# Kernel optimization log

Measured on AMD Instinct MI355X. Metric: run time of the kernel, lower is better.

Reference implementation:

```python
import jax, jax.numpy as jnp
import numpy as np

D_H = 2048      # d_hidden
D_E = 1408      # d_expert (per routed expert)
E = 8           # n_routed_experts
K = 2           # n_experts_per_token (top-k)
N_SHARED = 2    # n_shared_experts -> shared expert dim = D_E * N_SHARED
B, S = 1, 2048
D_S = D_E * N_SHARED


def setup_inputs() -> dict:
    key = jax.random.key(0)
    ks = jax.random.split(key, 8)
    def init(k, shape, fan_in):
        # nn.Linear default init: U(-1/sqrt(fan_in), 1/sqrt(fan_in))
        bound = 1.0 / np.sqrt(fan_in)
        return jax.random.uniform(k, shape, jnp.float32, -bound, bound)
    x = jax.random.normal(ks[0], (B, S, D_H), jnp.float32)
    gate_W = init(ks[1], (E, D_H), D_H)          # router: logits = x @ gate_W.T
    Wg_e = init(ks[2], (E, D_E, D_H), D_H)       # per-expert W_gate (out,in)
    Wu_e = init(ks[3], (E, D_E, D_H), D_H)       # per-expert W_up
    Wd_e = init(ks[4], (E, D_H, D_E), D_E)       # per-expert W_down
    Wg_s = init(ks[5], (D_S, D_H), D_H)          # shared expert W_gate
    Wu_s = init(ks[6], (D_S, D_H), D_H)
    Wd_s = init(ks[7], (D_H, D_S), D_S)
    return {"x": x, "gate_W": gate_W, "Wg_e": Wg_e, "Wu_e": Wu_e,
            "Wd_e": Wd_e, "Wg_s": Wg_s, "Wu_s": Wu_s, "Wd_s": Wd_s}


def reference(x, gate_W, Wg_e, Wu_e, Wd_e, Wg_s, Wu_s, Wd_s):
    silu = jax.nn.silu
    # shared expert: SiLU-gated MLP over all tokens
    shared = (silu(x @ Wg_s.T) * (x @ Wu_s.T)) @ Wd_s.T          # [B,S,D_H]
    # gating: softmax over experts, then top-k scores/indices
    scores = jax.nn.softmax(x @ gate_W.T, axis=-1)                # [B,S,E]
    topk_scores, topk_idx = jax.lax.top_k(scores, K)              # [B,S,K]
    # dense combine weights w[t,e] = topk score if e selected else 0
    # (equivalent to the torch argsort-dispatch + scatter_reduce sum combine)
    w = jnp.sum(jax.nn.one_hot(topk_idx, E, dtype=x.dtype) * topk_scores[..., None], axis=-2)  # [B,S,E]
    xf = x.reshape(-1, D_H)                                       # [T,D_H], T = B*S
    wf = w.reshape(-1, E)                                         # [T,E]
    # per-expert SiLU-gated MLP, batched over experts
    g = jnp.einsum('td,efd->etf', xf, Wg_e)                       # [E,T,D_E]
    u = jnp.einsum('td,efd->etf', xf, Wu_e)
    h = silu(g) * u
    oe = jnp.einsum('etf,edf->etd', h, Wd_e)                      # [E,T,D_H]
    routed = jnp.einsum('etd,te->td', oe, wf).reshape(B, S, D_H)
    return routed + shared
```

## Files before the change

### kernel.cpp

```cpp
#include <hip/hip_runtime.h>

using short8 = __attribute__((ext_vector_type(8))) short;
using f32x4  = __attribute__((ext_vector_type(4))) float;
typedef unsigned short ushort_t;
typedef unsigned int u32;

#define T_TOK 2048
#define DH 2048
#define DE 1408
#define DS 2816
#define GU_NB 440
#define DN_NB 256

#define NGEc 23068672UL
#define NGSc 5767168UL
#define PA_CVT_BLOCKS 30208
#define PB_CVT_BLOCKS 7040

__device__ __forceinline__ unsigned short f2bf(float f) {
  unsigned u = __float_as_uint(f);
  u += 0x7FFF + ((u >> 16) & 1);
  return (unsigned short)(u >> 16);
}

__device__ __forceinline__ void gl_lds16(const void* g, void* l) {
  __builtin_amdgcn_global_load_lds((const __attribute__((address_space(1))) u32*)g,
                                   (__attribute__((address_space(3))) u32*)l, 16, 0, 0);
}

__device__ __forceinline__ short8 pack_bf8(float4 a, float4 b) {
  short8 o;
  o[0] = (short)f2bf(a.x); o[1] = (short)f2bf(a.y);
  o[2] = (short)f2bf(a.z); o[3] = (short)f2bf(a.w);
  o[4] = (short)f2bf(b.x); o[5] = (short)f2bf(b.y);
  o[6] = (short)f2bf(b.z); o[7] = (short)f2bf(b.w);
  return o;
}

__global__ void phaseA_kernel(const float* __restrict__ x, const float* __restrict__ gW,
                              int* __restrict__ counts, int* __restrict__ tok_e,
                              int* __restrict__ tok_slot, float* __restrict__ tok_w,
                              const float* __restrict__ Wg_e, const float* __restrict__ Wu_e,
                              const float* __restrict__ Wg_s, const float* __restrict__ Wu_s,
                              ushort_t* wbg_e, ushort_t* wbu_e,
                              ushort_t* wbg_s, ushort_t* wbu_s, ushort_t* xb) {
  int b = blockIdx.x;
  int tid = threadIdx.x;
  if (b < 512) {
    int wid = tid >> 6, lane = tid & 63;
    int t = b * 4 + wid;
    float acc[8] = {0.f,0.f,0.f,0.f,0.f,0.f,0.f,0.f};
    const float* xt = x + (size_t)t * DH;
    for (int i = lane; i < DH; i += 64) {
      float xv = xt[i];
#pragma unroll
      for (int e = 0; e < 8; e++) acc[e] += xv * gW[e * DH + i];
    }
#pragma unroll
    for (int e = 0; e < 8; e++) {
#pragma unroll
      for (int off = 32; off > 0; off >>= 1) acc[e] += __shfl_xor(acc[e], off);
    }
    if (lane == 0) {
      float mx = acc[0];
      for (int e = 1; e < 8; e++) mx = fmaxf(mx, acc[e]);
      float p[8], se = 0.f;
      for (int e = 0; e < 8; e++) { p[e] = __expf(acc[e] - mx); se += p[e]; }
      for (int e = 0; e < 8; e++) p[e] /= se;
      int i1 = 0;
      for (int e = 1; e < 8; e++) if (p[e] > p[i1]) i1 = e;
      int i2 = (i1 == 0) ? 1 : 0;
      for (int e = 0; e < 8; e++) if (e != i1 && p[e] > p[i2]) i2 = e;
      int s1 = atomicAdd(&counts[i1], 1);
      int s2 = atomicAdd(&counts[i2], 1);
      tok_e[2 * t] = i1;     tok_e[2 * t + 1] = i2;
      tok_slot[2 * t] = s1;  tok_slot[2 * t + 1] = s2;
      tok_w[2 * t] = p[i1];  tok_w[2 * t + 1] = p[i2];
    }
    return;
  }
  size_t i = (size_t)(b - 512) * 2048 + (size_t)tid * 8;
  const float* s; ushort_t* d; size_t o;
  if      (i < NGEc)                    { s = Wg_e; d = wbg_e; o = i; }
  else if (i < 2 * NGEc)                { s = Wu_e; d = wbu_e; o = i - NGEc; }
  else if (i < 2 * NGEc + NGSc)         { s = Wg_s; d = wbg_s; o = i - 2 * NGEc; }
  else if (i < 2 * NGEc + 2 * NGSc)     { s = Wu_s; d = wbu_s; o = i - 2 * NGEc - NGSc; }
  else                                  { s = x;    d = xb;    o = i - 2 * NGEc - 2 * NGSc; }
  float4 a = *(const float4*)(s + o);
  float4 bb = *(const float4*)(s + o + 4);
  *(short8*)(d + o) = pack_bf8(a, bb);
}

__global__ void prefix_assign_kernel(const int* __restrict__ counts, int* __restrict__ ebase,
                                     int* __restrict__ gu_off, int* __restrict__ dn_off,
                                     const int* __restrict__ tok_e, int* __restrict__ tok_slot,
                                     int* __restrict__ slot2tok) {
  __shared__ int sbase[8];
  if (threadIdx.x == 0) {
    int a = 0;
    for (int e = 0; e < 8; e++) { sbase[e] = a; ebase[e] = a; a += counts[e]; }
    int g = 0, d = 0;
    for (int z = 0; z < 8; z++) {
      gu_off[z] = g; dn_off[z] = d;
      int Lg = (counts[z] + 255) >> 8;
      g += Lg * 11;
      int Ld = (counts[z] + 255) >> 8;
      d += Ld * 8;
    }
    gu_off[8] = g; g += 88;
    gu_off[9] = g; g += 88;
    gu_off[10] = g;
    dn_off[8] = d; d += 64;
    dn_off[9] = d;
  }
  __syncthreads();
  for (int idx = threadIdx.x; idx < T_TOK * 2; idx += blockDim.x) {
    int e = tok_e[idx];
    int g = sbase[e] + tok_slot[idx];
    tok_slot[idx] = g;
    slot2tok[g] = idx >> 1;
  }
}

__global__ __launch_bounds__(512, 1) void phaseB_kernel(
    const ushort_t* __restrict__ xb, const int* __restrict__ counts,
    const int* __restrict__ ebase, const int* __restrict__ gu_off,
    const int* __restrict__ slot2tok,
    const ushort_t* __restrict__ Wbg_e, const ushort_t* __restrict__ Wbu_e,
    const ushort_t* __restrict__ Wbg_s, const ushort_t* __restrict__ Wbu_s,
    ushort_t* __restrict__ h_r, ushort_t* __restrict__ h_s,
    const float* __restrict__ Wd_e, const float* __restrict__ Wd_s,
    ushort_t* wbd_e, ushort_t* wbd_s) {
  extern __shared__ char smem[];
  int tid = threadIdx.x;
  if (blockIdx.x >= GU_NB) {
    size_t i = (size_t)(blockIdx.x - GU_NB) * 4096 + (size_t)tid * 8;
    const float* s; ushort_t* d; size_t o;
    if (i < NGEc) { s = Wd_e; d = wbd_e; o = i; }
    else          { s = Wd_s; d = wbd_s; o = i - NGEc; }
    float4 a = *(const float4*)(s + o);
    float4 bb = *(const float4*)(s + o + 4);
    *(short8*)(d + o) = pack_bf8(a, bb);
    return;
  }
  int b = blockIdx.x;
  int c = (b & 7) * (GU_NB >> 3) + (b >> 3);
  int off[11];
#pragma unroll
  for (int zz = 0; zz < 11; zz++) off[zz] = gu_off[zz];
  if (c >= off[10]) return;
  int z = 0;
#pragma unroll
  for (int zz = 1; zz < 10; zz++) if (c >= off[zz]) z = zz;
  int cz = c - off[z];

  bool routed = (z < 8);
  int cnt, gbase, Lm;
  const ushort_t *Bg, *Bu;
  if (routed) {
    cnt = counts[z]; gbase = ebase[z];
    Lm = (cnt + 255) >> 8;
    Bg = Wbg_e + (size_t)z * DE * DH;
    Bu = Wbu_e + (size_t)z * DE * DH;
  } else {
    cnt = T_TOK; gbase = 0; Lm = 8;
    Bg = Wbg_s + (size_t)(z - 8) * 1408 * DH;
    Bu = Wbu_s + (size_t)(z - 8) * 1408 * DH;
  }
  int mt = cz % Lm, y = cz / Lm;
  int m0 = mt * 256, n0 = y * 128;

  int lane = tid & 63, w = tid >> 6;
  int lr = lane & 15, lk = lane >> 4;
  int wm = w >> 1, wn = w & 1;

  const ushort_t* asrc[4];
  int adst[4];
#pragma unroll
  for (int j = 0; j < 4; j++) {
    int r = (w * 4 + j) * 8 + (lane >> 3);
    int lrow = m0 + r;
    int tok = routed ? ((lrow < cnt) ? slot2tok[gbase + lrow] : 0) : lrow;
    int cs = (lane & 7) ^ (r & 7);
    asrc[j] = xb + (size_t)tok * DH + cs * 8;
    adst[j] = (w * 4 + j) * 1024;
  }
  const ushort_t* gsrc[2];
  const ushort_t* usrc[2];
  int wdst[2];
#pragma unroll
  for (int j = 0; j < 2; j++) {
    int r = (w * 2 + j) * 8 + (lane >> 3);
    int cs = (lane & 7) ^ (r & 7);
    gsrc[j] = Bg + (size_t)(n0 + r) * DH + cs * 8;
    usrc[j] = Bu + (size_t)(n0 + r) * DH + cs * 8;
    wdst[j] = (w * 2 + j) * 1024;
  }

  f32x4 accg[4][4] = {};
  f32x4 accu[4][4] = {};

#define GU_STAGE(buf, k0)                                             \
  {                                                                   \
    char* ab = smem + (buf) * 32768;                                  \
    char* gb = smem + 65536 + (buf) * 16384;                          \
    char* ub = smem + 98304 + (buf) * 16384;                          \
    _Pragma("unroll")                                                 \
    for (int j = 0; j < 4; j++) gl_lds16(asrc[j] + (k0), ab + adst[j]); \
    _Pragma("unroll")                                                 \
    for (int j = 0; j < 2; j++) {                                     \
      gl_lds16(gsrc[j] + (k0), gb + wdst[j]);                         \
      gl_lds16(usrc[j] + (k0), ub + wdst[j]);                         \
    }                                                                 \
  }

  const int nt = DH >> 6;
  GU_STAGE(0, 0);
  __syncthreads();
  int cur = 0;
  for (int t = 0; t < nt; t++) {
    if (t + 1 < nt) GU_STAGE(cur ^ 1, (t + 1) * 64);
    const char* ab = smem + cur * 32768;
    const char* gb = smem + 65536 + cur * 16384;
    const char* ub = smem + 98304 + cur * 16384;
    short8 af[4][2], bg[4][2], bu[4][2];
#pragma unroll
    for (int m = 0; m < 4; m++) {
#pragma unroll
      for (int ks = 0; ks < 2; ks++) {
        int rr = wm * 64 + m * 16 + lr;
        af[m][ks] = *(const short8*)(ab + rr * 128 + ((ks * 64 + lk * 16) ^ ((rr & 7) << 4)));
      }
    }
#pragma unroll
    for (int n = 0; n < 4; n++) {
#pragma unroll
      for (int ks = 0; ks < 2; ks++) {
        int cc = wn * 64 + n * 16 + lr;
        bg[n][ks] = *(const short8*)(gb + cc * 128 + ((ks * 64 + lk * 16) ^ ((cc & 7) << 4)));
        bu[n][ks] = *(const short8*)(ub + cc * 128 + ((ks * 64 + lk * 16) ^ ((cc & 7) << 4)));
      }
    }
    __builtin_amdgcn_s_setprio(1);
#pragma unroll
    for (int m = 0; m < 4; m++) {
#pragma unroll
      for (int n = 0; n < 4; n++) {
#pragma unroll
        for (int ks = 0; ks < 2; ks++) {
          accg[m][n] = __builtin_amdgcn_mfma_f32_16x16x32_bf16(af[m][ks], bg[n][ks], accg[m][n], 0, 0, 0);
          accu[m][n] = __builtin_amdgcn_mfma_f32_16x16x32_bf16(af[m][ks], bu[n][ks], accu[m][n], 0, 0, 0);
        }
      }
    }
    __builtin_amdgcn_s_setprio(0);
    __syncthreads();
    cur ^= 1;
  }
#pragma unroll
  for (int m = 0; m < 4; m++) {
    int rowl = m0 + wm * 64 + m * 16 + lk * 4;
#pragma unroll
    for (int n = 0; n < 4; n++) {
      int col = n0 + wn * 64 + n * 16 + lr;
#pragma unroll
      for (int j = 0; j < 4; j++) {
        float g = accg[m][n][j], u = accu[m][n][j];
        float s = g / (1.f + __expf(-g));
        unsigned short hv = f2bf(s * u);
        if (routed) {
          if (rowl + j < cnt) h_r[(size_t)(gbase + rowl + j) * DE + col] = hv;
        } else {
          h_s[(size_t)(rowl + j) * DS + (z - 8) * 1408 + col] = hv;
        }
      }
    }
  }
}

__global__ __launch_bounds__(512, 1) void down_kernel(
    const ushort_t* __restrict__ h_r, const ushort_t* __restrict__ h_s,
    const int* __restrict__ counts, const int* __restrict__ ebase,
    const int* __restrict__ dn_off,
    const ushort_t* __restrict__ Wbd_e, const ushort_t* __restrict__ Wbd_s,
    float* __restrict__ oe, float* __restrict__ out) {
  extern __shared__ char smem[];

  int b = blockIdx.x;
  int c = (b & 7) * (DN_NB >> 3) + (b >> 3);
  int off[10];
#pragma unroll
  for (int zz = 0; zz < 10; zz++) off[zz] = dn_off[zz];
  if (c >= off[9]) return;
  int z = 0;
#pragma unroll
  for (int zz = 1; zz < 9; zz++) if (c >= off[zz]) z = zz;
  int cz = c - off[z];

  bool routed = (z < 8);
  int cnt, gbase, K, Lm;
  const ushort_t* Abase;
  const ushort_t* Bw;
  if (routed) {
    cnt = counts[z]; gbase = ebase[z];
    Lm = (cnt + 255) >> 8;
    K = DE;
    Abase = h_r + (size_t)gbase * DE;
    Bw = Wbd_e + (size_t)z * DH * DE;
  } else {
    cnt = T_TOK; gbase = 0; Lm = 8;
    K = DS;
    Abase = h_s;
    Bw = Wbd_s;
  }
  int mt = cz % Lm, y = cz / Lm;
  int m0 = mt * 256, n0 = y * 256;

  int tid = threadIdx.x;
  int lane = tid & 63, w = tid >> 6;
  int lr = lane & 15, lk = lane >> 4;
  int wm = w >> 2, wn = w & 3;

  const ushort_t* asrc[4];
  const ushort_t* bsrc[4];
  int dst4[4];
#pragma unroll
  for (int j = 0; j < 4; j++) {
    int r = (w * 4 + j) * 8 + (lane >> 3);
    int cs = (lane & 7) ^ (r & 7);
    asrc[j] = Abase + (size_t)(m0 + r) * K + cs * 8;
    bsrc[j] = Bw + (size_t)(n0 + r) * K + cs * 8;
    dst4[j] = (w * 4 + j) * 1024;
  }

  f32x4 acc[8][4] = {};

#define DN_STAGE(buf, k0)                                             \
  {                                                                   \
    char* ab = smem + (buf) * 32768;                                  \
    char* wb2 = smem + 65536 + (buf) * 32768;                         \
    _Pragma("unroll")                                                 \
    for (int j = 0; j < 4; j++) {                                     \
      gl_lds16(asrc[j] + (k0), ab + dst4[j]);                         \
      gl_lds16(bsrc[j] + (k0), wb2 + dst4[j]);                        \
    }                                                                 \
  }

  const int nt = K >> 6;
  DN_STAGE(0, 0);
  __syncthreads();
  int cur = 0;
  for (int t = 0; t < nt; t++) {
    if (t + 1 < nt) DN_STAGE(cur ^ 1, (t + 1) * 64);
    const char* ab = smem + cur * 32768;
    const char* wb2 = smem + 65536 + cur * 32768;
    short8 bf[4][2];
#pragma unroll
    for (int n = 0; n < 4; n++) {
#pragma unroll
      for (int ks = 0; ks < 2; ks++) {
        int cc = wn * 64 + n * 16 + lr;
        bf[n][ks] = *(const short8*)(wb2 + cc * 128 + ((ks * 64 + lk * 16) ^ ((cc & 7) << 4)));
      }
    }
    __builtin_amdgcn_s_setprio(1);
#pragma unroll
    for (int mh = 0; mh < 2; mh++) {
      short8 af[4][2];
#pragma unroll
      for (int m4 = 0; m4 < 4; m4++) {
#pragma unroll
        for (int ks = 0; ks < 2; ks++) {
          int rr = wm * 128 + (mh * 4 + m4) * 16 + lr;
          af[m4][ks] = *(const short8*)(ab + rr * 128 + ((ks * 64 + lk * 16) ^ ((rr & 7) << 4)));
        }
      }
#pragma unroll
      for (int m4 = 0; m4 < 4; m4++) {
#pragma unroll
        for (int n = 0; n < 4; n++) {
#pragma unroll
          for (int ks = 0; ks < 2; ks++) {
            acc[mh * 4 + m4][n] = __builtin_amdgcn_mfma_f32_16x16x32_bf16(
                af[m4][ks], bf[n][ks], acc[mh * 4 + m4][n], 0, 0, 0);
          }
        }
      }
    }
    __builtin_amdgcn_s_setprio(0);
    __syncthreads();
    cur ^= 1;
  }
#pragma unroll
  for (int m = 0; m < 8; m++) {
    int rowl = m0 + wm * 128 + m * 16 + lk * 4;
#pragma unroll
    for (int n = 0; n < 4; n++) {
      int col = n0 + wn * 64 + n * 16 + lr;
#pragma unroll
      for (int j = 0; j < 4; j++) {
        if (routed) {
          if (rowl + j < cnt) oe[(size_t)(gbase + rowl + j) * DH + col] = acc[m][n][j];
        } else {
          out[(size_t)(rowl + j) * DH + col] = acc[m][n][j];
        }
      }
    }
  }
}

__global__ void combine_kernel(const int* __restrict__ tok_gslot,
                               const float* __restrict__ tok_w,
                               const float* __restrict__ oe,
                               float* __restrict__ out) {
  int t = blockIdx.x;
  int g1 = tok_gslot[2 * t], g2 = tok_gslot[2 * t + 1];
  float w1 = tok_w[2 * t], w2 = tok_w[2 * t + 1];
  int i = threadIdx.x * 8;
  const float4* p1 = (const float4*)(oe + (size_t)g1 * DH + i);
  const float4* p2 = (const float4*)(oe + (size_t)g2 * DH + i);
  float4* po = (float4*)(out + (size_t)t * DH + i);
  float4 a0 = p1[0], a1 = p1[1];
  float4 b0 = p2[0], b1 = p2[1];
  float4 o0 = po[0], o1 = po[1];
  o0.x += w1 * a0.x + w2 * b0.x;  o0.y += w1 * a0.y + w2 * b0.y;
  o0.z += w1 * a0.z + w2 * b0.z;  o0.w += w1 * a0.w + w2 * b0.w;
  o1.x += w1 * a1.x + w2 * b1.x;  o1.y += w1 * a1.y + w2 * b1.y;
  o1.z += w1 * a1.z + w2 * b1.z;  o1.w += w1 * a1.w + w2 * b1.w;
  po[0] = o0; po[1] = o1;
}

extern "C" void kernel_launch(void* const* d_in, const int* in_sizes, int n_in,
                              void* d_out, int out_size, void* d_ws, size_t ws_size,
                              hipStream_t stream) {
  const float* x    = (const float*)d_in[0];
  const float* gW   = (const float*)d_in[1];
  const float* Wg_e = (const float*)d_in[2];
  const float* Wu_e = (const float*)d_in[3];
  const float* Wd_e = (const float*)d_in[4];
  const float* Wg_s = (const float*)d_in[5];
  const float* Wu_s = (const float*)d_in[6];
  const float* Wd_s = (const float*)d_in[7];
  float* out = (float*)d_out;

  char* ws = (char*)d_ws;
  int*   counts   = (int*)ws;
  int*   ebase    = (int*)(ws + 64);
  int*   gu_off   = (int*)(ws + 128);
  int*   dn_off   = (int*)(ws + 192);
  int*   tok_e    = (int*)(ws + 256);
  int*   tok_slot = (int*)(ws + 256 + 16384);
  float* tok_w    = (float*)(ws + 256 + 32768);
  int*   slot2tok = (int*)(ws + 256 + 49152);
  ushort_t* xb  = (ushort_t*)(ws + 131072);
  ushort_t* h_r = (ushort_t*)(ws + 131072 + (size_t)T_TOK * DH * 2);
  ushort_t* h_s = h_r + (size_t)4096 * DE;
  float*    oe  = (float*)((char*)h_s + (size_t)T_TOK * DS * 2);
  ushort_t* wb  = (ushort_t*)((char*)oe + (size_t)4096 * DH * 4);
  ushort_t* wbg_e = wb;
  ushort_t* wbu_e = wb + NGEc;
  ushort_t* wbd_e = wb + 2 * NGEc;
  ushort_t* wbg_s = wb + 3 * NGEc;
  ushort_t* wbu_s = wbg_s + NGSc;
  ushort_t* wbd_s = wbg_s + 2 * NGSc;

  hipFuncSetAttribute((const void*)phaseB_kernel,
                      hipFuncAttributeMaxDynamicSharedMemorySize, 131072);
  hipFuncSetAttribute((const void*)down_kernel,
                      hipFuncAttributeMaxDynamicSharedMemorySize, 131072);

  hipMemsetAsync(counts, 0, 64, stream);
  phaseA_kernel<<<512 + PA_CVT_BLOCKS, 256, 0, stream>>>(
      x, gW, counts, tok_e, tok_slot, tok_w,
      Wg_e, Wu_e, Wg_s, Wu_s, wbg_e, wbu_e, wbg_s, wbu_s, xb);
  prefix_assign_kernel<<<1, 256, 0, stream>>>(counts, ebase, gu_off, dn_off,
                                              tok_e, tok_slot, slot2tok);
  phaseB_kernel<<<GU_NB + PB_CVT_BLOCKS, 512, 131072, stream>>>(
      xb, counts, ebase, gu_off, slot2tok, wbg_e, wbu_e, wbg_s, wbu_s, h_r, h_s,
      Wd_e, Wd_s, wbd_e, wbd_s);
  down_kernel<<<DN_NB, 512, 131072, stream>>>(
      h_r, h_s, counts, ebase, dn_off, wbd_e, wbd_s, oe, out);
  combine_kernel<<<T_TOK, 256, 0, stream>>>(tok_slot, tok_w, oe, out);
}
```

Before: 343.9 us.

## Split GEMM mainloops into four barrier-synchronized phases with interleaved async loads

```diff
diff --git a/kernel.cpp b/kernel.cpp
--- a/kernel.cpp
+++ b/kernel.cpp
@@ -16,6 +16,8 @@
 #define NGSc 5767168UL
 #define PA_CVT_BLOCKS 30208
 #define PB_CVT_BLOCKS 7040
+
+#define FENCE() asm volatile("" ::: "memory")
 
 __device__ __forceinline__ unsigned short f2bf(float f) {
   unsigned u = __float_as_uint(f);
@@ -174,16 +176,19 @@
   int lr = lane & 15, lk = lane >> 4;
   int wm = w >> 1, wn = w & 1;
 
-  const ushort_t* asrc[4];
-  int adst[4];
-#pragma unroll
-  for (int j = 0; j < 4; j++) {
-    int r = (w * 4 + j) * 8 + (lane >> 3);
-    int lrow = m0 + r;
-    int tok = routed ? ((lrow < cnt) ? slot2tok[gbase + lrow] : 0) : lrow;
-    int cs = (lane & 7) ^ (r & 7);
-    asrc[j] = xb + (size_t)tok * DH + cs * 8;
-    adst[j] = (w * 4 + j) * 1024;
+  const ushort_t* asrc[2][2];
+  int adst[2][2];
+#pragma unroll
+  for (int h = 0; h < 2; h++) {
+#pragma unroll
+    for (int j = 0; j < 2; j++) {
+      int r = h * 128 + (w * 2 + j) * 8 + (lane >> 3);
+      int lrow = m0 + r;
+      int tok = routed ? ((lrow < cnt) ? slot2tok[gbase + lrow] : 0) : lrow;
+      int cs = (lane & 7) ^ (r & 7);
+      asrc[h][j] = xb + (size_t)tok * DH + cs * 8;
+      adst[h][j] = h * 16384 + (w * 2 + j) * 1024;
+    }
   }
   const ushort_t* gsrc[2];
   const ushort_t* usrc[2];
@@ -200,62 +205,82 @@
   f32x4 accg[4][4] = {};
   f32x4 accu[4][4] = {};
 
-#define GU_STAGE(buf, k0)                                             \
-  {                                                                   \
-    char* ab = smem + (buf) * 32768;                                  \
-    char* gb = smem + 65536 + (buf) * 16384;                          \
-    char* ub = smem + 98304 + (buf) * 16384;                          \
-    _Pragma("unroll")                                                 \
-    for (int j = 0; j < 4; j++) gl_lds16(asrc[j] + (k0), ab + adst[j]); \
-    _Pragma("unroll")                                                 \
-    for (int j = 0; j < 2; j++) {                                     \
-      gl_lds16(gsrc[j] + (k0), gb + wdst[j]);                         \
-      gl_lds16(usrc[j] + (k0), ub + wdst[j]);                         \
-    }                                                                 \
-  }
+#define GU_ST_A(p, h, k0)                                              \
+  { char* _d = smem + (p) * 32768;                                     \
+    gl_lds16(asrc[h][0] + (k0), _d + adst[h][0]);                      \
+    gl_lds16(asrc[h][1] + (k0), _d + adst[h][1]); }
+#define GU_ST_G(p, k0)                                                 \
+  { char* _d = smem + 65536 + (p) * 16384;                             \
+    gl_lds16(gsrc[0] + (k0), _d + wdst[0]);                            \
+    gl_lds16(gsrc[1] + (k0), _d + wdst[1]); }
+#define GU_ST_U(p, k0)                                                 \
+  { char* _d = smem + 98304 + (p) * 16384;                             \
+    gl_lds16(usrc[0] + (k0), _d + wdst[0]);                            \
+    gl_lds16(usrc[1] + (k0), _d + wdst[1]); }
 
   const int nt = DH >> 6;
-  GU_STAGE(0, 0);
-  __syncthreads();
-  int cur = 0;
+  GU_ST_A(0, 0, 0); GU_ST_A(0, 1, 0);
+  GU_ST_G(0, 0);    GU_ST_U(0, 0);
+  GU_ST_G(1, 64);   GU_ST_U(1, 64);
+  asm volatile("s_waitcnt vmcnt(4)" ::: "memory");
+  FENCE(); __builtin_amdgcn_s_barrier(); FENCE();
+
+  short8 bfr[4][2];
   for (int t = 0; t < nt; t++) {
-    if (t + 1 < nt) GU_STAGE(cur ^ 1, (t + 1) * 64);
-    const char* ab = smem + cur * 32768;
-    const char* gb = smem + 65536 + cur * 16384;
-    const char* ub = smem + 98304 + cur * 16384;
-    short8 af[4][2], bg[4][2], bu[4][2];
-#pragma unroll
-    for (int m = 0; m < 4; m++) {
-#pragma unroll
-      for (int ks = 0; ks < 2; ks++) {
-        int rr = wm * 64 + m * 16 + lr;
-        af[m][ks] = *(const short8*)(ab + rr * 128 + ((ks * 64 + lk * 16) ^ ((rr & 7) << 4)));
-      }
-    }
-#pragma unroll
-    for (int n = 0; n < 4; n++) {
-#pragma unroll
-      for (int ks = 0; ks < 2; ks++) {
-        int cc = wn * 64 + n * 16 + lr;
-        bg[n][ks] = *(const short8*)(gb + cc * 128 + ((ks * 64 + lk * 16) ^ ((cc & 7) << 4)));
-        bu[n][ks] = *(const short8*)(ub + cc * 128 + ((ks * 64 + lk * 16) ^ ((cc & 7) << 4)));
-      }
-    }
-    __builtin_amdgcn_s_setprio(1);
-#pragma unroll
-    for (int m = 0; m < 4; m++) {
-#pragma unroll
-      for (int n = 0; n < 4; n++) {
+    int p = t & 1;
+    const char* ab = smem + p * 32768;
+    const char* gb = smem + 65536 + p * 16384;
+    const char* ub = smem + 98304 + p * 16384;
+    int k1 = (t + 1) * 64, k2 = (t + 2) * 64;
+#pragma unroll
+    for (int ph = 0; ph < 4; ph++) {
+      if (ph == 0 || ph == 2) {
+        const char* wbp = (ph == 0) ? gb : ub;
+#pragma unroll
+        for (int n = 0; n < 4; n++) {
+#pragma unroll
+          for (int ks = 0; ks < 2; ks++) {
+            int cc = wn * 64 + n * 16 + lr;
+            bfr[n][ks] = *(const short8*)(wbp + cc * 128 + ((ks * 64 + lk * 16) ^ ((cc & 7) << 4)));
+          }
+        }
+      }
+      short8 af[2][2];
+#pragma unroll
+      for (int m2 = 0; m2 < 2; m2++) {
 #pragma unroll
         for (int ks = 0; ks < 2; ks++) {
-          accg[m][n] = __builtin_amdgcn_mfma_f32_16x16x32_bf16(af[m][ks], bg[n][ks], accg[m][n], 0, 0, 0);
-          accu[m][n] = __builtin_amdgcn_mfma_f32_16x16x32_bf16(af[m][ks], bu[n][ks], accu[m][n], 0, 0, 0);
-        }
-      }
-    }
-    __builtin_amdgcn_s_setprio(0);
-    __syncthreads();
-    cur ^= 1;
+          int rr = wm * 64 + (ph & 1) * 32 + m2 * 16 + lr;
+          af[m2][ks] = *(const short8*)(ab + rr * 128 + ((ks * 64 + lk * 16) ^ ((rr & 7) << 4)));
+        }
+      }
+      if      (ph == 0) { if (t + 1 < nt) GU_ST_A(p ^ 1, 0, k1); }
+      else if (ph == 1) { if (t + 1 < nt) GU_ST_A(p ^ 1, 1, k1); }
+      else if (ph == 2) { if (t + 2 < nt) GU_ST_G(p, k2); }
+      else {
+        if (t + 2 < nt) { GU_ST_U(p, k2); asm volatile("s_waitcnt vmcnt(4)" ::: "memory"); }
+        else            {                 asm volatile("s_waitcnt vmcnt(0)" ::: "memory"); }
+      }
+      FENCE(); __builtin_amdgcn_s_barrier(); FENCE();
+      __builtin_amdgcn_s_setprio(1);
+#pragma unroll
+      for (int m2 = 0; m2 < 2; m2++) {
+#pragma unroll
+        for (int n = 0; n < 4; n++) {
+#pragma unroll
+          for (int ks = 0; ks < 2; ks++) {
+            if (ph < 2)
+              accg[(ph & 1) * 2 + m2][n] = __builtin_amdgcn_mfma_f32_16x16x32_bf16(
+                  af[m2][ks], bfr[n][ks], accg[(ph & 1) * 2 + m2][n], 0, 0, 0);
+            else
+              accu[(ph & 1) * 2 + m2][n] = __builtin_amdgcn_mfma_f32_16x16x32_bf16(
+                  af[m2][ks], bfr[n][ks], accu[(ph & 1) * 2 + m2][n], 0, 0, 0);
+          }
+        }
+      }
+      __builtin_amdgcn_s_setprio(0);
+      FENCE(); __builtin_amdgcn_s_barrier(); FENCE();
+    }
   }
 #pragma unroll
   for (int m = 0; m < 4; m++) {
@@ -321,75 +346,89 @@
   int lr = lane & 15, lk = lane >> 4;
   int wm = w >> 2, wn = w & 3;
 
-  const ushort_t* asrc[4];
-  const ushort_t* bsrc[4];
-  int dst4[4];
-#pragma unroll
-  for (int j = 0; j < 4; j++) {
-    int r = (w * 4 + j) * 8 + (lane >> 3);
-    int cs = (lane & 7) ^ (r & 7);
-    asrc[j] = Abase + (size_t)(m0 + r) * K + cs * 8;
-    bsrc[j] = Bw + (size_t)(n0 + r) * K + cs * 8;
-    dst4[j] = (w * 4 + j) * 1024;
+  const ushort_t* asrc[2][2];
+  const ushort_t* bsrc[2][2];
+  int sdst[2][2];
+#pragma unroll
+  for (int h = 0; h < 2; h++) {
+#pragma unroll
+    for (int j = 0; j < 2; j++) {
+      int r = h * 128 + (w * 2 + j) * 8 + (lane >> 3);
+      int cs = (lane & 7) ^ (r & 7);
+      asrc[h][j] = Abase + (size_t)(m0 + r) * K + cs * 8;
+      bsrc[h][j] = Bw + (size_t)(n0 + r) * K + cs * 8;
+      sdst[h][j] = h * 16384 + (w * 2 + j) * 1024;
+    }
   }
 
   f32x4 acc[8][4] = {};
 
-#define DN_STAGE(buf, k0)                                             \
-  {                                                                   \
-    char* ab = smem + (buf) * 32768;                                  \
-    char* wb2 = smem + 65536 + (buf) * 32768;                         \
-    _Pragma("unroll")                                                 \
-    for (int j = 0; j < 4; j++) {                                     \
-      gl_lds16(asrc[j] + (k0), ab + dst4[j]);                         \
-      gl_lds16(bsrc[j] + (k0), wb2 + dst4[j]);                        \
-    }                                                                 \
-  }
+#define DN_ST_A(p, h, k0)                                              \
+  { char* _d = smem + (p) * 32768;                                     \
+    gl_lds16(asrc[h][0] + (k0), _d + sdst[h][0]);                      \
+    gl_lds16(asrc[h][1] + (k0), _d + sdst[h][1]); }
+#define DN_ST_B(p, h, k0)                                              \
+  { char* _d = smem + 65536 + (p) * 32768;                             \
+    gl_lds16(bsrc[h][0] + (k0), _d + sdst[h][0]);                      \
+    gl_lds16(bsrc[h][1] + (k0), _d + sdst[h][1]); }
 
   const int nt = K >> 6;
-  DN_STAGE(0, 0);
-  __syncthreads();
-  int cur = 0;
+  DN_ST_A(0, 0, 0); DN_ST_A(0, 1, 0);
+  DN_ST_B(0, 0, 0); DN_ST_B(0, 1, 0);
+  DN_ST_B(1, 0, 64); DN_ST_B(1, 1, 64);
+  asm volatile("s_waitcnt vmcnt(4)" ::: "memory");
+  FENCE(); __builtin_amdgcn_s_barrier(); FENCE();
+
+  short8 bfr[4][2];
   for (int t = 0; t < nt; t++) {
-    if (t + 1 < nt) DN_STAGE(cur ^ 1, (t + 1) * 64);
-    const char* ab = smem + cur * 32768;
-    const char* wb2 = smem + 65536 + cur * 32768;
-    short8 bf[4][2];
-#pragma unroll
-    for (int n = 0; n < 4; n++) {
-#pragma unroll
-      for (int ks = 0; ks < 2; ks++) {
-        int cc = wn * 64 + n * 16 + lr;
-        bf[n][ks] = *(const short8*)(wb2 + cc * 128 + ((ks * 64 + lk * 16) ^ ((cc & 7) << 4)));
-      }
-    }
-    __builtin_amdgcn_s_setprio(1);
-#pragma unroll
-    for (int mh = 0; mh < 2; mh++) {
-      short8 af[4][2];
-#pragma unroll
-      for (int m4 = 0; m4 < 4; m4++) {
+    int p = t & 1;
+    const char* ab = smem + p * 32768;
+    const char* bb = smem + 65536 + p * 32768;
+    int k1 = (t + 1) * 64, k2 = (t + 2) * 64;
+#pragma unroll
+    for (int ph = 0; ph < 4; ph++) {
+      if (ph == 0) {
+#pragma unroll
+        for (int n = 0; n < 4; n++) {
+#pragma unroll
+          for (int ks = 0; ks < 2; ks++) {
+            int cc = wn * 64 + n * 16 + lr;
+            bfr[n][ks] = *(const short8*)(bb + cc * 128 + ((ks * 64 + lk * 16) ^ ((cc & 7) << 4)));
+          }
+        }
+      }
+      short8 af[2][2];
+#pragma unroll
+      for (int m2 = 0; m2 < 2; m2++) {
 #pragma unroll
         for (int ks = 0; ks < 2; ks++) {
-          int rr = wm * 128 + (mh * 4 + m4) * 16 + lr;
-          af[m4][ks] = *(const short8*)(ab + rr * 128 + ((ks * 64 + lk * 16) ^ ((rr & 7) << 4)));
-        }
-      }
-#pragma unroll
-      for (int m4 = 0; m4 < 4; m4++) {
+          int rr = wm * 128 + ph * 32 + m2 * 16 + lr;
+          af[m2][ks] = *(const short8*)(ab + rr * 128 + ((ks * 64 + lk * 16) ^ ((rr & 7) << 4)));
+        }
+      }
+      if      (ph == 0) { if (t + 1 < nt) DN_ST_A(p ^ 1, 0, k1); }
+      else if (ph == 1) { if (t + 1 < nt) DN_ST_A(p ^ 1, 1, k1); }
+      else if (ph == 2) { if (t + 2 < nt) DN_ST_B(p, 0, k2); }
+      else {
+        if (t + 2 < nt) { DN_ST_B(p, 1, k2); asm volatile("s_waitcnt vmcnt(4)" ::: "memory"); }
+        else            {                    asm volatile("s_waitcnt vmcnt(0)" ::: "memory"); }
+      }
+      FENCE(); __builtin_amdgcn_s_barrier(); FENCE();
+      __builtin_amdgcn_s_setprio(1);
+#pragma unroll
+      for (int m2 = 0; m2 < 2; m2++) {
 #pragma unroll
         for (int n = 0; n < 4; n++) {
 #pragma unroll
           for (int ks = 0; ks < 2; ks++) {
-            acc[mh * 4 + m4][n] = __builtin_amdgcn_mfma_f32_16x16x32_bf16(
-                af[m4][ks], bf[n][ks], acc[mh * 4 + m4][n], 0, 0, 0);
+            acc[ph * 2 + m2][n] = __builtin_amdgcn_mfma_f32_16x16x32_bf16(
+                af[m2][ks], bfr[n][ks], acc[ph * 2 + m2][n], 0, 0, 0);
           }
         }
       }
-    }
-    __builtin_amdgcn_s_setprio(0);
-    __syncthreads();
-    cur ^= 1;
+      __builtin_amdgcn_s_setprio(0);
+      FENCE(); __builtin_amdgcn_s_barrier(); FENCE();
+    }
   }
 #pragma unroll
   for (int m = 0; m < 8; m++) {
```

Result: no change. 343.4 us (-0.1%).

## Interleave down-proj LDS loads into 4-phase MFMA loop and grid-stride weight conversion

Applied to the files above, without the earlier changes.

```diff
diff --git a/kernel.cpp b/kernel.cpp
--- a/kernel.cpp
+++ b/kernel.cpp
@@ -14,8 +14,11 @@
 
 #define NGEc 23068672UL
 #define NGSc 5767168UL
-#define PA_CVT_BLOCKS 30208
+#define NXc  4194304UL
+#define PA_CVT_BLOCKS 3584
 #define PB_CVT_BLOCKS 7040
+
+#define FENCE() asm volatile("" ::: "memory")
 
 __device__ __forceinline__ unsigned short f2bf(float f) {
   unsigned u = __float_as_uint(f);
@@ -79,16 +82,21 @@
     }
     return;
   }
-  size_t i = (size_t)(b - 512) * 2048 + (size_t)tid * 8;
-  const float* s; ushort_t* d; size_t o;
-  if      (i < NGEc)                    { s = Wg_e; d = wbg_e; o = i; }
-  else if (i < 2 * NGEc)                { s = Wu_e; d = wbu_e; o = i - NGEc; }
-  else if (i < 2 * NGEc + NGSc)         { s = Wg_s; d = wbg_s; o = i - 2 * NGEc; }
-  else if (i < 2 * NGEc + 2 * NGSc)     { s = Wu_s; d = wbu_s; o = i - 2 * NGEc - NGSc; }
-  else                                  { s = x;    d = xb;    o = i - 2 * NGEc - 2 * NGSc; }
-  float4 a = *(const float4*)(s + o);
-  float4 bb = *(const float4*)(s + o + 4);
-  *(short8*)(d + o) = pack_bf8(a, bb);
+  const size_t NVEC = (2 * NGEc + 2 * NGSc + NXc) / 8;
+  size_t v0 = (size_t)(b - 512) * 256 + tid;
+  const size_t stride = (size_t)PA_CVT_BLOCKS * 256;
+  for (size_t v = v0; v < NVEC; v += stride) {
+    size_t i = v * 8;
+    const float* s; ushort_t* d; size_t o;
+    if      (i < NGEc)                    { s = Wg_e; d = wbg_e; o = i; }
+    else if (i < 2 * NGEc)                { s = Wu_e; d = wbu_e; o = i - NGEc; }
+    else if (i < 2 * NGEc + NGSc)         { s = Wg_s; d = wbg_s; o = i - 2 * NGEc; }
+    else if (i < 2 * NGEc + 2 * NGSc)     { s = Wu_s; d = wbu_s; o = i - 2 * NGEc - NGSc; }
+    else                                  { s = x;    d = xb;    o = i - 2 * NGEc - 2 * NGSc; }
+    float4 a = *(const float4*)(s + o);
+    float4 bb = *(const float4*)(s + o + 4);
+    __builtin_nontemporal_store(pack_bf8(a, bb), (short8*)(d + o));
+  }
 }
 
 __global__ void prefix_assign_kernel(const int* __restrict__ counts, int* __restrict__ ebase,
@@ -140,7 +148,7 @@
     else          { s = Wd_s; d = wbd_s; o = i - NGEc; }
     float4 a = *(const float4*)(s + o);
     float4 bb = *(const float4*)(s + o + 4);
-    *(short8*)(d + o) = pack_bf8(a, bb);
+    __builtin_nontemporal_store(pack_bf8(a, bb), (short8*)(d + o));
     return;
   }
   int b = blockIdx.x;
@@ -321,75 +329,89 @@
   int lr = lane & 15, lk = lane >> 4;
   int wm = w >> 2, wn = w & 3;
 
-  const ushort_t* asrc[4];
-  const ushort_t* bsrc[4];
-  int dst4[4];
-#pragma unroll
-  for (int j = 0; j < 4; j++) {
-    int r = (w * 4 + j) * 8 + (lane >> 3);
-    int cs = (lane & 7) ^ (r & 7);
-    asrc[j] = Abase + (size_t)(m0 + r) * K + cs * 8;
-    bsrc[j] = Bw + (size_t)(n0 + r) * K + cs * 8;
-    dst4[j] = (w * 4 + j) * 1024;
+  const ushort_t* asrc[2][2];
+  const ushort_t* bsrc[2][2];
+  int sdst[2][2];
+#pragma unroll
+  for (int h = 0; h < 2; h++) {
+#pragma unroll
+    for (int j = 0; j < 2; j++) {
+      int r = h * 128 + (w * 2 + j) * 8 + (lane >> 3);
+      int cs = (lane & 7) ^ (r & 7);
+      asrc[h][j] = Abase + (size_t)(m0 + r) * K + cs * 8;
+      bsrc[h][j] = Bw + (size_t)(n0 + r) * K + cs * 8;
+      sdst[h][j] = h * 16384 + (w * 2 + j) * 1024;
+    }
   }
 
   f32x4 acc[8][4] = {};
 
-#define DN_STAGE(buf, k0)                                             \
-  {                                                                   \
-    char* ab = smem + (buf) * 32768;                                  \
-    char* wb2 = smem + 65536 + (buf) * 32768;                         \
-    _Pragma("unroll")                                                 \
-    for (int j = 0; j < 4; j++) {                                     \
-      gl_lds16(asrc[j] + (k0), ab + dst4[j]);                         \
-      gl_lds16(bsrc[j] + (k0), wb2 + dst4[j]);                        \
-    }                                                                 \
-  }
+#define DN_ST_A(p, h, k0)                                              \
+  { char* _d = smem + (p) * 32768;                                     \
+    gl_lds16(asrc[h][0] + (k0), _d + sdst[h][0]);                      \
+    gl_lds16(asrc[h][1] + (k0), _d + sdst[h][1]); }
+#define DN_ST_B(p, h, k0)                                              \
+  { char* _d = smem + 65536 + (p) * 32768;                             \
+    gl_lds16(bsrc[h][0] + (k0), _d + sdst[h][0]);                      \
+    gl_lds16(bsrc[h][1] + (k0), _d + sdst[h][1]); }
 
   const int nt = K >> 6;
-  DN_STAGE(0, 0);
-  __syncthreads();
-  int cur = 0;
+  DN_ST_A(0, 0, 0); DN_ST_A(0, 1, 0);
+  DN_ST_B(0, 0, 0); DN_ST_B(0, 1, 0);
+  DN_ST_B(1, 0, 64); DN_ST_B(1, 1, 64);
+  asm volatile("s_waitcnt vmcnt(4)" ::: "memory");
+  FENCE(); __builtin_amdgcn_s_barrier(); FENCE();
+
+  short8 bfr[4][2];
   for (int t = 0; t < nt; t++) {
-    if (t + 1 < nt) DN_STAGE(cur ^ 1, (t + 1) * 64);
-    const char* ab = smem + cur * 32768;
-    const char* wb2 = smem + 65536 + cur * 32768;
-    short8 bf[4][2];
-#pragma unroll
-    for (int n = 0; n < 4; n++) {
-#pragma unroll
-      for (int ks = 0; ks < 2; ks++) {
-        int cc = wn * 64 + n * 16 + lr;
-        bf[n][ks] = *(const short8*)(wb2 + cc * 128 + ((ks * 64 + lk * 16) ^ ((cc & 7) << 4)));
-      }
-    }
-    __builtin_amdgcn_s_setprio(1);
-#pragma unroll
-    for (int mh = 0; mh < 2; mh++) {
-      short8 af[4][2];
-#pragma unroll
-      for (int m4 = 0; m4 < 4; m4++) {
-#pragma unroll
-        for (int ks = 0; ks < 2; ks++) {
-          int rr = wm * 128 + (mh * 4 + m4) * 16 + lr;
-          af[m4][ks] = *(const short8*)(ab + rr * 128 + ((ks * 64 + lk * 16) ^ ((rr & 7) << 4)));
-        }
-      }
-#pragma unroll
-      for (int m4 = 0; m4 < 4; m4++) {
+    int p = t & 1;
+    const char* ab = smem + p * 32768;
+    const char* bb = smem + 65536 + p * 32768;
+    int k1 = (t + 1) * 64, k2 = (t + 2) * 64;
+#pragma unroll
+    for (int ph = 0; ph < 4; ph++) {
+      if (ph == 0) {
 #pragma unroll
         for (int n = 0; n < 4; n++) {
 #pragma unroll
           for (int ks = 0; ks < 2; ks++) {
-            acc[mh * 4 + m4][n] = __builtin_amdgcn_mfma_f32_16x16x32_bf16(
-                af[m4][ks], bf[n][ks], acc[mh * 4 + m4][n], 0, 0, 0);
+            int cc = wn * 64 + n * 16 + lr;
+            bfr[n][ks] = *(const short8*)(bb + cc * 128 + ((ks * 64 + lk * 16) ^ ((cc & 7) << 4)));
           }
         }
       }
-    }
-    __builtin_amdgcn_s_setprio(0);
-    __syncthreads();
-    cur ^= 1;
+      short8 af[2][2];
+#pragma unroll
+      for (int m2 = 0; m2 < 2; m2++) {
+#pragma unroll
+        for (int ks = 0; ks < 2; ks++) {
+          int rr = wm * 128 + ph * 32 + m2 * 16 + lr;
+          af[m2][ks] = *(const short8*)(ab + rr * 128 + ((ks * 64 + lk * 16) ^ ((rr & 7) << 4)));
+        }
+      }
+      if      (ph == 0) { if (t + 1 < nt) DN_ST_A(p ^ 1, 0, k1); }
+      else if (ph == 1) { if (t + 1 < nt) DN_ST_A(p ^ 1, 1, k1); }
+      else if (ph == 2) { if (t + 2 < nt) DN_ST_B(p, 0, k2); }
+      else {
+        if (t + 2 < nt) { DN_ST_B(p, 1, k2); asm volatile("s_waitcnt vmcnt(4)" ::: "memory"); }
+        else            {                    asm volatile("s_waitcnt vmcnt(0)" ::: "memory"); }
+      }
+      FENCE(); __builtin_amdgcn_s_barrier(); FENCE();
+      __builtin_amdgcn_s_setprio(1);
+#pragma unroll
+      for (int m2 = 0; m2 < 2; m2++) {
+#pragma unroll
+        for (int n = 0; n < 4; n++) {
+#pragma unroll
+          for (int ks = 0; ks < 2; ks++) {
+            acc[ph * 2 + m2][n] = __builtin_amdgcn_mfma_f32_16x16x32_bf16(
+                af[m2][ks], bfr[n][ks], acc[ph * 2 + m2][n], 0, 0, 0);
+          }
+        }
+      }
+      __builtin_amdgcn_s_setprio(0);
+      FENCE(); __builtin_amdgcn_s_barrier(); FENCE();
+    }
   }
 #pragma unroll
   for (int m = 0; m < 8; m++) {
```

Measured after the change: 353.8 us. 2.9% more time.
